# Kernel optimization log

Measured on AMD Instinct MI355X. Metric: run time of the kernel, lower is better.

Reference implementation:

```python
import jax, jax.numpy as jnp
import numpy as np

H, W = 512, 512          # output image size (RenderLayer h, w)
CHUNK = 16               # faces per scan step in the rasterizer
BIG = 1e30
EPS = 1e-8


def _edge(ax, ay, bx, by, px, py):
    # 2D edge function (signed parallelogram area)
    return (px - ax) * (by - ay) - (py - ay) * (bx - ax)


def _project(v, campos, camrot, focal, princpt):
    # v: [N,V,3] -> camera space and pixel space (x_pix, y_pix, z_cam)
    v_cam = jnp.einsum('nij,nvj->nvi', camrot, v - campos[:, None])
    z = jnp.maximum(v_cam[..., 2:3], EPS)
    xy = jnp.einsum('nij,nvj->nvi', focal, v_cam[..., :2] / z) + princpt[:, None]
    v_pix = jnp.concatenate([xy, v_cam[..., 2:3]], axis=-1)
    return v_cam, v_pix


def _rasterize(v_pix, vi):
    # Z-buffer rasterization: returns per-pixel face index (-1 = background).
    N = v_pix.shape[0]
    F = vi.shape[0]
    px = jnp.arange(W, dtype=v_pix.dtype)[None, None, None, :]
    py = jnp.arange(H, dtype=v_pix.dtype)[None, None, :, None]
    tri = v_pix[:, vi]                       # [N,F,3,3]
    nchunks = F // CHUNK
    tri_c = jnp.moveaxis(tri.reshape(N, nchunks, CHUNK, 3, 3), 1, 0)  # [nc,N,C,3,3]
    base = jnp.arange(nchunks, dtype=jnp.int32) * CHUNK

    def body(carry, xs):
        best_d, best_i = carry
        t, b0 = xs                           # t: [N,C,3,3]
        x0 = t[:, :, 0, 0][..., None, None]; y0 = t[:, :, 0, 1][..., None, None]; z0 = t[:, :, 0, 2][..., None, None]
        x1 = t[:, :, 1, 0][..., None, None]; y1 = t[:, :, 1, 1][..., None, None]; z1 = t[:, :, 1, 2][..., None, None]
        x2 = t[:, :, 2, 0][..., None, None]; y2 = t[:, :, 2, 1][..., None, None]; z2 = t[:, :, 2, 2][..., None, None]
        w0 = _edge(x1, y1, x2, y2, px, py)   # [N,C,H,W]
        w1 = _edge(x2, y2, x0, y0, px, py)
        w2 = _edge(x0, y0, x1, y1, px, py)
        area = _edge(x0, y0, x1, y1, x2, y2)
        inside = (w0 * area >= 0) & (w1 * area >= 0) & (w2 * area >= 0) & (jnp.abs(area) > EPS)
        sa = jnp.where(jnp.abs(area) > EPS, area, 1.0)
        zi = (w0 / sa) / jnp.maximum(z0, EPS) + (w1 / sa) / jnp.maximum(z1, EPS) + (w2 / sa) / jnp.maximum(z2, EPS)
        valid = inside & (z0 > EPS) & (z1 > EPS) & (z2 > EPS) & (zi > EPS)
        d = jnp.where(valid, 1.0 / jnp.maximum(zi, EPS), BIG)
        d_min = jnp.min(d, axis=1)
        i_min = jnp.argmin(d, axis=1).astype(jnp.int32) + b0
        upd = d_min < best_d
        return (jnp.where(upd, d_min, best_d), jnp.where(upd, i_min, best_i)), None

    init = (jnp.full((N, H, W), BIG, v_pix.dtype), jnp.full((N, H, W), -1, jnp.int32))
    (best_d, best_i), _ = jax.lax.scan(body, init, (tri_c, base))
    mask = best_d < BIG
    return jnp.where(mask, best_i, -1), mask


def _interp(v_pix, vt, vi, vti, index_img, mask):
    # Perspective-correct barycentric interp of depth and texcoords (interp_vert_attrs)
    safe = jnp.maximum(index_img, 0)
    f_v = vi[safe]                            # [N,H,W,3]
    f_vt = vti[safe]
    pv = jax.vmap(lambda vp, t: vp[t])(v_pix, f_v)  # [N,H,W,3,3]
    px = jnp.arange(W, dtype=v_pix.dtype)[None, None, :]
    py = jnp.arange(H, dtype=v_pix.dtype)[None, :, None]
    x0, y0 = pv[..., 0, 0], pv[..., 0, 1]
    x1, y1 = pv[..., 1, 0], pv[..., 1, 1]
    x2, y2 = pv[..., 2, 0], pv[..., 2, 1]
    w0 = _edge(x1, y1, x2, y2, px, py)
    w1 = _edge(x2, y2, x0, y0, px, py)
    w2 = _edge(x0, y0, x1, y1, px, py)
    area = _edge(x0, y0, x1, y1, x2, y2)
    sa = jnp.where(jnp.abs(area) > EPS, area, 1.0)
    b = jnp.stack([w0, w1, w2], -1) / sa[..., None]     # screen-space bary [N,H,W,3]
    z = jnp.maximum(pv[..., 2], EPS)
    bz = b / z
    zi = jnp.maximum(jnp.sum(bz, -1, keepdims=True), EPS)
    bary = jnp.where(mask[..., None], bz / zi, 0.0)     # perspective-correct bary
    depth_img = jnp.where(mask, 1.0 / zi[..., 0], 0.0)
    vt_tri = vt[f_vt]                                   # [N,H,W,3,2]
    vt_img = jnp.einsum('nhwk,nhwkc->nhwc', bary, vt_tri)
    return depth_img, bary, vt_img


def _grid_sample_border(tex, grid):
    # torch.nn.functional.grid_sample: bilinear, padding_mode='border', align_corners=False
    N, C, Ht, Wt = tex.shape
    t = jnp.moveaxis(tex, 1, -1)              # [N,Ht,Wt,C]
    ix = (grid[..., 0] + 1.0) * 0.5 * Wt - 0.5
    iy = (grid[..., 1] + 1.0) * 0.5 * Ht - 0.5
    x0 = jnp.floor(ix); y0 = jnp.floor(iy)
    fx = (ix - x0)[..., None]; fy = (iy - y0)[..., None]
    x0i = jnp.clip(x0.astype(jnp.int32), 0, Wt - 1)
    x1i = jnp.clip(x0.astype(jnp.int32) + 1, 0, Wt - 1)
    y0i = jnp.clip(y0.astype(jnp.int32), 0, Ht - 1)
    y1i = jnp.clip(y0.astype(jnp.int32) + 1, 0, Ht - 1)
    gather = jax.vmap(lambda img, y, x: img[y, x])
    v00 = gather(t, y0i, x0i); v01 = gather(t, y0i, x1i)
    v10 = gather(t, y1i, x0i); v11 = gather(t, y1i, x1i)
    out = (v00 * (1 - fx) + v01 * fx) * (1 - fy) + (v10 * (1 - fx) + v11 * fx) * fy
    return jnp.moveaxis(out, -1, 1)           # [N,C,H,W]


def setup_inputs() -> dict:
    key = jax.random.key(0)
    ks = jax.random.split(key, 6)
    N, V, F, T = 2, 4096, 2048, 4096
    xy = jax.random.uniform(ks[0], (N, V, 2), minval=-1.0, maxval=1.0)
    z = jax.random.uniform(ks[1], (N, V, 1), minval=2.0, maxval=4.0)
    v = jnp.concatenate([xy, z], -1)
    tex = jax.random.normal(ks[2], (N, 3, 1024, 1024), dtype=jnp.float32)
    vt = jax.random.uniform(ks[3], (T, 2))
    vi = jax.random.randint(ks[4], (F, 3), 0, V, dtype=jnp.int32)
    vti = jax.random.randint(ks[5], (F, 3), 0, T, dtype=jnp.int32)
    campos = jnp.zeros((N, 3), jnp.float32)
    camrot = jnp.tile(jnp.eye(3, dtype=jnp.float32)[None], (N, 1, 1))
    focal = jnp.tile(jnp.array([[512.0, 0.0], [0.0, 512.0]], jnp.float32)[None], (N, 1, 1))
    princpt = jnp.full((N, 2), 256.0, jnp.float32)
    return {"v": v, "tex": tex, "vt": vt, "vi": vi, "vti": vti,
            "campos": campos, "camrot": camrot, "focal": focal, "princpt": princpt}


def reference(v, tex, vt, vi, vti, campos, camrot, focal, princpt):
    vt = vt.at[:, 1].set(1.0 - vt[:, 1])      # flip_uvs=True buffer transform
    v_cam, v_pix = _project(v, campos, camrot, focal, princpt)
    index_img, mask = _rasterize(jax.lax.stop_gradient(v_pix), vi)
    depth_img, bary, vt_img = _interp(v_pix, vt, vi, vti, index_img, mask)
    grid = vt_img * 2.0 - 1.0                 # uv in [0,1] -> grid_sample coords
    render = _grid_sample_border(tex, grid) * mask[:, None].astype(tex.dtype)
    bary_img = jnp.moveaxis(bary, -1, 1)
    return render, mask.astype(jnp.float32), depth_img, vt_img, bary_img, index_img
```

## Files before the change

kernel.cpp:

```cpp
#include <hip/hip_runtime.h>
#include <math.h>

#define EPSD 1e-8
#define EPSF 1e-8f
#define IMG_H 512
#define IMG_W 512
#define TEX_W 1024
#define TEX_H 1024
#define REJ_SLACK 1e-3
#define FULL_THR 16.0
#define TILES_X (IMG_W / 16)
#define TILES_Y (IMG_H / 16)
#define TILES_PER_IMG (TILES_X * TILES_Y)

__global__ __launch_bounds__(256) void k_project(
    const float* __restrict__ v,
    const float* __restrict__ campos,
    const float* __restrict__ camrot,
    const float* __restrict__ focal,
    const float* __restrict__ princpt,
    double* __restrict__ vpixd,
    int N, int V) {
#pragma clang fp contract(off)
  int i = blockIdx.x * blockDim.x + threadIdx.x;
  if (i >= N * V) return;
  int n = i / V;
  const float* vv = v + (size_t)i * 3;
  double ax = (double)vv[0] - (double)campos[n * 3 + 0];
  double ay = (double)vv[1] - (double)campos[n * 3 + 1];
  double az = (double)vv[2] - (double)campos[n * 3 + 2];
  const float* R = camrot + (size_t)n * 9;
  double cx = ((double)R[0] * ax + (double)R[1] * ay) + (double)R[2] * az;
  double cy = ((double)R[3] * ax + (double)R[4] * ay) + (double)R[5] * az;
  double cz = ((double)R[6] * ax + (double)R[7] * ay) + (double)R[8] * az;
  double zz = fmax(cz, EPSD);
  double xd = cx / zz;
  double yd = cy / zz;
  const float* Fc = focal + (size_t)n * 4;
  double px = ((double)Fc[0] * xd + (double)Fc[1] * yd) + (double)princpt[n * 2 + 0];
  double py = ((double)Fc[2] * xd + (double)Fc[3] * yd) + (double)princpt[n * 2 + 1];
  vpixd[(size_t)i * 3 + 0] = px;
  vpixd[(size_t)i * 3 + 1] = py;
  vpixd[(size_t)i * 3 + 2] = cz;
}

__global__ __launch_bounds__(256) void k_setup(
    const double* __restrict__ vpixd,
    const int* __restrict__ vi,
    double2* __restrict__ tri,
    float4* __restrict__ bbox,
    int* __restrict__ counter,
    int N, int V, int F) {
#pragma clang fp contract(off)
  int i = blockIdx.x * blockDim.x + threadIdx.x;
  if (i == 0) counter[0] = 0;
  if (i >= N * F) return;
  int n = i / F;
  int f = i - n * F;
  int i0 = vi[f * 3 + 0], i1 = vi[f * 3 + 1], i2 = vi[f * 3 + 2];
  const double* p0 = vpixd + ((size_t)n * V + i0) * 3;
  const double* p1 = vpixd + ((size_t)n * V + i1) * 3;
  const double* p2 = vpixd + ((size_t)n * V + i2) * 3;
  double x0 = p0[0], y0 = p0[1], z0 = p0[2];
  double x1 = p1[0], y1 = p1[1], z1 = p1[2];
  double x2 = p2[0], y2 = p2[1], z2 = p2[2];
  double A0 = y2 - y1, B0 = x2 - x1;
  double A1 = y0 - y2, B1 = x0 - x2;
  double A2 = y1 - y0, B2 = x1 - x0;
  double area = (x2 - x0) * A2 - (y2 - y0) * B2;
  bool valid = (fabs(area) > EPSD) && (z0 > EPSD) && (z1 > EPSD) && (z2 > EPSD);
  double s = area;
  double EA0 = 0.0, EB0 = 0.0, EC0 = -1.0;
  double EA1 = 0.0, EB1 = 0.0, EC1 = -1.0;
  double EA2 = 0.0, EB2 = 0.0, EC2 = -1.0;
  double P = 0.0, Q = 0.0, S = 0.0;
  if (valid) {
    EA0 = A0 * s; EB0 = -(B0 * s); EC0 = (y1 * B0 - x1 * A0) * s;
    EA1 = A1 * s; EB1 = -(B1 * s); EC1 = (y2 * B1 - x2 * A1) * s;
    EA2 = A2 * s; EB2 = -(B2 * s); EC2 = (y0 * B2 - x0 * A2) * s;
    double s2 = s * s;
    double R0 = 1.0 / (s2 * fmax(z0, EPSD));
    double R1 = 1.0 / (s2 * fmax(z1, EPSD));
    double R2 = 1.0 / (s2 * fmax(z2, EPSD));
    P = EA0 * R0 + EA1 * R1 + EA2 * R2;
    S = EB0 * R0 + EB1 * R1 + EB2 * R2;
    Q = EC0 * R0 + EC1 * R1 + EC2 * R2;
  }
  double2* T = tri + (size_t)i * 6;
  T[0] = make_double2(EA0, EB0);
  T[1] = make_double2(EC0, EA1);
  T[2] = make_double2(EB1, EC1);
  T[3] = make_double2(EA2, EB2);
  T[4] = make_double2(EC2, P);
  T[5] = make_double2(Q, S);
  float mnx = (float)fmin(x0, fmin(x1, x2));
  float mny = (float)fmin(y0, fmin(y1, y2));
  float mxx = (float)fmax(x0, fmax(x1, x2));
  float mxy = (float)fmax(y0, fmax(y1, y2));
  bbox[i] = make_float4(mnx, mny, mxx, mxy);
}

__device__ inline void steal_to_tile(int s, int& tx, int& ty) {
  int k = (int)(__fsqrt_rn((float)s) * 0.5f);
  while (k > 0 && 4 * k * k > s) --k;
  while (4 * (k + 1) * (k + 1) <= s) ++k;
  int o = s - 4 * k * k;
  int L = 2 * k + 2;
  int x0 = TILES_X / 2 - 1 - k, y0 = TILES_Y / 2 - 1 - k;
  int side = o / (L - 1);
  int off = o - side * (L - 1);
  if (side == 0)      { tx = x0 + off;         ty = y0; }
  else if (side == 1) { tx = x0 + L - 1;       ty = y0 + off; }
  else if (side == 2) { tx = x0 + L - 1 - off; ty = y0 + L - 1; }
  else                { tx = x0;               ty = y0 + L - 1 - off; }
}

__device__ inline double rl_d(double v, int l) {
  int lo = __builtin_amdgcn_readlane(__double2loint(v), l);
  int hi = __builtin_amdgcn_readlane(__double2hiint(v), l);
  return __hiloint2double(hi, lo);
}

__global__ __launch_bounds__(256, 2) void k_raster(
    const double2* __restrict__ tri,
    const float4* __restrict__ bbox,
    int* __restrict__ counter,
    const double* __restrict__ vpixd,
    const float* __restrict__ vt,
    const int* __restrict__ vi,
    const int* __restrict__ vti,
    const float* __restrict__ tex,
    float* __restrict__ out,
    int N, int V, int F) {
#pragma clang fp contract(off)
  __shared__ __align__(16) char smem[12288];
  double* zbuf = (double*)smem;
  int* ibuf = (int*)(smem + 8192);
  __shared__ int s_steal;

  int tid = threadIdx.x;
  int w = tid >> 6, lane = tid & 63;
  int xl = lane & 15, yb = (lane >> 4) * 4;
  int FQ = (F + 3) >> 2;
  int fbeg = w * FQ;
  int fend = min(F, fbeg + FQ);
  int NR = (fend > fbeg) ? ((fend - fbeg + 63) >> 6) : 0;
  const int TOT = N * TILES_PER_IMG;
  const int HW = IMG_H * IMG_W;
  const size_t NHW = (size_t)N * HW;
  float* out_render = out;
  float* out_mask = out + 3 * NHW;
  float* out_depth = out + 4 * NHW;
  float* out_vt = out + 5 * NHW;
  float* out_bary = out + 7 * NHW;
  float* out_idx = out + 10 * NHW;

  for (;;) {
    if (tid == 0) s_steal = atomicAdd(counter, 1);
    __syncthreads();
    int s = s_steal;
    if (s >= TOT) break;
    int n = s % N;
    int q = s / N;
    int tx, ty;
    steal_to_tile(q, tx, ty);

    int x = tx * 16 + xl;
    int ytop = ty * 16;
    double px = (double)x;
    double py0 = (double)(ytop + yb);
    float tminx = (float)(tx * 16) - 0.5f;
    float tmaxx = tminx + 16.0f;
    float tminy = (float)ytop - 0.5f;
    float tmaxy = tminy + 16.0f;
    double X0 = (double)(tx * 16), X1 = X0 + 15.0;
    double Y0 = (double)ytop, Y1 = Y0 + 15.0;

    double bz[4];
    int bi[4];
#pragma unroll
    for (int r = 0; r < 4; ++r) { bz[r] = EPSD; bi[r] = -1; }

    const double2* trin = tri + (size_t)n * F * 6;
    const float4* bbn = bbox + (size_t)n * F;

    float4 bbB = make_float4(0.f, 0.f, 0.f, 0.f);
    bool bbpA = false;
    double2 A0, A1, A2, A3, A4, A5;
    if (NR > 0) {
      int t0 = fbeg + lane;
      float4 bbA;
      if (t0 < fend) bbA = bbn[t0];
      bbpA = (t0 < fend) &&
             !(bbA.z < tminx || bbA.x > tmaxx || bbA.w < tminy || bbA.y > tmaxy);
      if (bbpA) {
        const double2* T = trin + (size_t)t0 * 6;
        A0 = T[0]; A1 = T[1]; A2 = T[2]; A3 = T[3]; A4 = T[4]; A5 = T[5];
      }
      if (t0 + 64 < fend) bbB = bbn[t0 + 64];
    }
    for (int r = 0; r < NR; ++r) {
      int tbase = fbeg + (r << 6);
      bool surv = false, full = false;
      if (bbpA) {
        double xs0 = (A0.x >= 0.0) ? X1 : X0;
        double ys0 = (A0.y >= 0.0) ? Y1 : Y0;
        double w0M = fma(ys0, A0.y, fma(xs0, A0.x, A1.x));
        double xs1 = (A1.y >= 0.0) ? X1 : X0;
        double ys1 = (A2.x >= 0.0) ? Y1 : Y0;
        double w1M = fma(ys1, A2.x, fma(xs1, A1.y, A2.y));
        double xs2 = (A3.x >= 0.0) ? X1 : X0;
        double ys2 = (A3.y >= 0.0) ? Y1 : Y0;
        double w2M = fma(ys2, A3.y, fma(xs2, A3.x, A4.x));
        surv = (w0M >= -REJ_SLACK) & (w1M >= -REJ_SLACK) & (w2M >= -REJ_SLACK);
        if (surv) {
          double xn0 = (A0.x >= 0.0) ? X0 : X1;
          double yn0 = (A0.y >= 0.0) ? Y0 : Y1;
          double w0m = fma(yn0, A0.y, fma(xn0, A0.x, A1.x));
          double xn1 = (A1.y >= 0.0) ? X0 : X1;
          double yn1 = (A2.x >= 0.0) ? Y0 : Y1;
          double w1m = fma(yn1, A2.x, fma(xn1, A1.y, A2.y));
          double xn2 = (A3.x >= 0.0) ? X0 : X1;
          double yn2 = (A3.y >= 0.0) ? Y0 : Y1;
          double w2m = fma(yn2, A3.y, fma(xn2, A3.x, A4.x));
          full = (w0m >= FULL_THR) & (w1m >= FULL_THR) & (w2m >= FULL_THR);
        }
      }
      unsigned long long m = __ballot(surv);
      unsigned long long mf = __ballot(surv && full);
      int tn1 = tbase + 64 + lane;
      bool bbpB = (tn1 < fend) &&
                  !(bbB.z < tminx || bbB.x > tmaxx || bbB.w < tminy || bbB.y > tmaxy);
      double2 B0, B1, B2, B3, B4, B5;
      if (bbpB) {
        const double2* T = trin + (size_t)tn1 * 6;
        B0 = T[0]; B1 = T[1]; B2 = T[2]; B3 = T[3]; B4 = T[4]; B5 = T[5];
      }
      if (tn1 + 64 < fend) bbB = bbn[tn1 + 64];
      while (m) {
        int src = (int)__builtin_ctzll(m);
        m &= m - 1;
        int ti = tbase + src;
        double P = rl_d(A4.y, src);
        double Qq = rl_d(A5.x, src);
        double S = rl_d(A5.y, src);
        double uu = fma(px, P, Qq);
        if ((mf >> src) & 1ull) {
          double py = py0;
#pragma unroll
          for (int rr = 0; rr < 4; ++rr) {
            double zi = fma(py, S, uu);
            if (zi > bz[rr]) { bz[rr] = zi; bi[rr] = ti; }
            py += 1.0;
          }
        } else {
          double EA0 = rl_d(A0.x, src), EB0 = rl_d(A0.y, src);
          double EC0 = rl_d(A1.x, src), EA1 = rl_d(A1.y, src);
          double EB1 = rl_d(A2.x, src), EC1 = rl_d(A2.y, src);
          double EA2 = rl_d(A3.x, src), EB2 = rl_d(A3.y, src);
          double EC2 = rl_d(A4.x, src);
          double q0 = fma(px, EA0, EC0);
          double q1 = fma(px, EA1, EC1);
          double q2 = fma(px, EA2, EC2);
          double py = py0;
#pragma unroll
          for (int rr = 0; rr < 4; ++rr) {
            double W0 = fma(py, EB0, q0);
            double W1 = fma(py, EB1, q1);
            double W2 = fma(py, EB2, q2);
            double zi = fma(py, S, uu);
            int msk = (__double2hiint(W0) | __double2hiint(W1) |
                       __double2hiint(W2)) >> 31;
            zi = __hiloint2double(__double2hiint(zi) | msk, __double2loint(zi));
            if (zi > bz[rr]) { bz[rr] = zi; bi[rr] = ti; }
            py += 1.0;
          }
        }
      }
      A0 = B0; A1 = B1; A2 = B2; A3 = B3; A4 = B4; A5 = B5;
      bbpA = bbpB;
    }

    __syncthreads();
#pragma unroll
    for (int r = 0; r < 4; ++r) {
      int pix = (yb + r) * 16 + xl;
      zbuf[w * 256 + pix] = bz[r];
      ibuf[w * 256 + pix] = bi[r];
    }
    __syncthreads();
    {
      int pix = tid;
      double z = zbuf[pix];
      int i = ibuf[pix];
#pragma unroll
      for (int qq = 1; qq < 4; ++qq) {
        double zq = zbuf[qq * 256 + pix];
        int iq = ibuf[qq * 256 + pix];
        bool take = (zq > z) || ((zq == z) && ((unsigned)iq < (unsigned)i));
        if (take) { z = zq; i = iq; }
      }
      int yloc = pix >> 4, xloc = pix & 15;
      int y = ytop + yloc;
      int xg = tx * 16 + xloc;
      int p = y * IMG_W + xg;
      size_t gid = (size_t)n * HW + p;
      out_idx[gid] = (float)i;

      int idx = i;
      if (idx < 0) {
        for (int c = 0; c < 3; ++c) out_render[(size_t)(n * 3 + c) * HW + p] = 0.0f;
        out_mask[gid] = 0.0f;
        out_depth[gid] = 0.0f;
        out_vt[(size_t)gid * 2 + 0] = 0.0f;
        out_vt[(size_t)gid * 2 + 1] = 0.0f;
        for (int k = 0; k < 3; ++k) out_bary[(size_t)(n * 3 + k) * HW + p] = 0.0f;
      } else {
        int f0 = vi[idx * 3 + 0], f1 = vi[idx * 3 + 1], f2 = vi[idx * 3 + 2];
        int t0i = vti[idx * 3 + 0], t1i = vti[idx * 3 + 1], t2i = vti[idx * 3 + 2];
        const double* pv0 = vpixd + ((size_t)n * V + f0) * 3;
        const double* pv1 = vpixd + ((size_t)n * V + f1) * 3;
        const double* pv2 = vpixd + ((size_t)n * V + f2) * 3;
        float x0 = (float)pv0[0], y0 = (float)pv0[1], z0 = (float)pv0[2];
        float x1 = (float)pv1[0], y1 = (float)pv1[1], z1 = (float)pv1[2];
        float x2 = (float)pv2[0], y2 = (float)pv2[1], z2 = (float)pv2[2];
        float pxf = (float)xg, pyf = (float)y;
        float w0 = (pxf - x1) * (y2 - y1) - (pyf - y1) * (x2 - x1);
        float w1 = (pxf - x2) * (y0 - y2) - (pyf - y2) * (x0 - x2);
        float w2 = (pxf - x0) * (y1 - y0) - (pyf - y0) * (x1 - x0);
        float area = (x2 - x0) * (y1 - y0) - (y2 - y0) * (x1 - x0);
        float sa = (fabsf(area) > EPSF) ? area : 1.0f;
        float b0 = w0 / sa, b1 = w1 / sa, b2 = w2 / sa;
        float zz0 = fmaxf(z0, EPSF), zz1 = fmaxf(z1, EPSF), zz2 = fmaxf(z2, EPSF);
        float bz0 = b0 / zz0, bz1 = b1 / zz1, bz2 = b2 / zz2;
        float zi = fmaxf((bz0 + bz1) + bz2, EPSF);
        float r0 = bz0 / zi, r1 = bz1 / zi, r2 = bz2 / zi;
        float depth = 1.0f / zi;
        float u0 = vt[(size_t)t0i * 2 + 0], q0 = 1.0f - vt[(size_t)t0i * 2 + 1];
        float u1 = vt[(size_t)t1i * 2 + 0], q1 = 1.0f - vt[(size_t)t1i * 2 + 1];
        float u2 = vt[(size_t)t2i * 2 + 0], q2 = 1.0f - vt[(size_t)t2i * 2 + 1];
        float vtx = (r0 * u0 + r1 * u1) + r2 * u2;
        float vty = (r0 * q0 + r1 * q1) + r2 * q2;
        float gx = vtx * 2.0f - 1.0f;
        float gy = vty * 2.0f - 1.0f;
        float ix = ((gx + 1.0f) * 0.5f) * (float)TEX_W - 0.5f;
        float iy = ((gy + 1.0f) * 0.5f) * (float)TEX_H - 0.5f;
        float x0f = floorf(ix), y0f = floorf(iy);
        float fx = ix - x0f, fy = iy - y0f;
        int x0i = min(max((int)x0f, 0), TEX_W - 1);
        int x1i = min(max((int)x0f + 1, 0), TEX_W - 1);
        int y0i = min(max((int)y0f, 0), TEX_H - 1);
        int y1i = min(max((int)y0f + 1, 0), TEX_H - 1);
        float omfx = 1.0f - fx, omfy = 1.0f - fy;
        for (int c = 0; c < 3; ++c) {
          const float* tc = tex + (size_t)(n * 3 + c) * TEX_H * TEX_W;
          float v00 = tc[(size_t)y0i * TEX_W + x0i];
          float v01 = tc[(size_t)y0i * TEX_W + x1i];
          float v10 = tc[(size_t)y1i * TEX_W + x0i];
          float v11 = tc[(size_t)y1i * TEX_W + x1i];
          float o = (v00 * omfx + v01 * fx) * omfy + (v10 * omfx + v11 * fx) * fy;
          out_render[(size_t)(n * 3 + c) * HW + p] = o;
        }
        out_mask[gid] = 1.0f;
        out_depth[gid] = depth;
        out_vt[(size_t)gid * 2 + 0] = vtx;
        out_vt[(size_t)gid * 2 + 1] = vty;
        out_bary[(size_t)(n * 3 + 0) * HW + p] = r0;
        out_bary[(size_t)(n * 3 + 1) * HW + p] = r1;
        out_bary[(size_t)(n * 3 + 2) * HW + p] = r2;
      }
    }
  }
}

extern "C" void kernel_launch(void* const* d_in, const int* in_sizes, int n_in,
                              void* d_out, int out_size, void* d_ws, size_t ws_size,
                              hipStream_t stream) {
  const float* v = (const float*)d_in[0];
  const float* tex = (const float*)d_in[1];
  const float* vt = (const float*)d_in[2];
  const int* vi = (const int*)d_in[3];
  const int* vti = (const int*)d_in[4];
  const float* campos = (const float*)d_in[5];
  const float* camrot = (const float*)d_in[6];
  const float* focal = (const float*)d_in[7];
  const float* princpt = (const float*)d_in[8];
  int N = in_sizes[5] / 3;
  int V = in_sizes[0] / (3 * N);
  int F = in_sizes[3] / 3;

  char* wp = (char*)d_ws;
  double* vpixd = (double*)wp;
  wp += sizeof(double) * (size_t)N * V * 3;
  double2* tri = (double2*)wp;
  wp += sizeof(double2) * (size_t)N * F * 6;
  float4* bbox = (float4*)wp;
  wp += sizeof(float4) * (size_t)N * F;
  int* counter = (int*)wp;

  int nv = N * V;
  k_project<<<(nv + 255) / 256, 256, 0, stream>>>(v, campos, camrot, focal,
                                                  princpt, vpixd, N, V);
  int nf = N * F;
  k_setup<<<(nf + 255) / 256, 256, 0, stream>>>(vpixd, vi, tri, bbox, counter,
                                                N, V, F);
  int nblk = 1024;
  int tot = N * TILES_PER_IMG;
  if (nblk > tot) nblk = tot;
  k_raster<<<nblk, 256, 0, stream>>>(tri, bbox, counter, vpixd, vt, vi, vti,
                                     tex, (float*)d_out, N, V, F);
}
```

Before: 168.0 us.

## Enlarge raster tiles to 32x16 with center-out separable tile ordering

Raster tiles grow from 16x16 to 32x16. Each lane now covers 8 rows instead of 4, and the shared-memory z/index merge buffers are doubled to match. This amortises per-triangle work (bbox test, triangle loads, readlane broadcasts) over more pixels per tile. The spiral tile ordering is replaced with a simpler center-out permutation applied separately to each axis, and the block count rises. The cost is more registers per thread and more shared memory, and larger tiles overlap more triangles, so more partial-coverage work is done per tile.

```diff
diff --git a/kernel.cpp b/kernel.cpp
--- a/kernel.cpp
+++ b/kernel.cpp
@@ -9,8 +9,10 @@
 #define TEX_H 1024
 #define REJ_SLACK 1e-3
 #define FULL_THR 16.0
-#define TILES_X (IMG_W / 16)
-#define TILES_Y (IMG_H / 16)
+#define TILE_W 32
+#define TILE_H 16
+#define TILES_X (IMG_W / TILE_W)
+#define TILES_Y (IMG_H / TILE_H)
 #define TILES_PER_IMG (TILES_X * TILES_Y)
 
 __global__ __launch_bounds__(256) void k_project(
@@ -100,19 +102,9 @@
   bbox[i] = make_float4(mnx, mny, mxx, mxy);
 }
 
-__device__ inline void steal_to_tile(int s, int& tx, int& ty) {
-  int k = (int)(__fsqrt_rn((float)s) * 0.5f);
-  while (k > 0 && 4 * k * k > s) --k;
-  while (4 * (k + 1) * (k + 1) <= s) ++k;
-  int o = s - 4 * k * k;
-  int L = 2 * k + 2;
-  int x0 = TILES_X / 2 - 1 - k, y0 = TILES_Y / 2 - 1 - k;
-  int side = o / (L - 1);
-  int off = o - side * (L - 1);
-  if (side == 0)      { tx = x0 + off;         ty = y0; }
-  else if (side == 1) { tx = x0 + L - 1;       ty = y0 + off; }
-  else if (side == 2) { tx = x0 + L - 1 - off; ty = y0 + L - 1; }
-  else                { tx = x0;               ty = y0 + L - 1 - off; }
+__device__ inline int perm_co(int i, int n) {
+  int h = n >> 1;
+  return (i & 1) ? (h - 1 - (i >> 1)) : (h + (i >> 1));
 }
 
 __device__ inline double rl_d(double v, int l) {
@@ -133,14 +125,14 @@
     float* __restrict__ out,
     int N, int V, int F) {
 #pragma clang fp contract(off)
-  __shared__ __align__(16) char smem[12288];
+  __shared__ __align__(16) char smem[24576];
   double* zbuf = (double*)smem;
-  int* ibuf = (int*)(smem + 8192);
+  int* ibuf = (int*)(smem + 16384);
   __shared__ int s_steal;
 
   int tid = threadIdx.x;
   int w = tid >> 6, lane = tid & 63;
-  int xl = lane & 15, yb = (lane >> 4) * 4;
+  int xl = lane & 31, yb = (lane >> 5) * 8;
   int FQ = (F + 3) >> 2;
   int fbeg = w * FQ;
   int fend = min(F, fbeg + FQ);
@@ -162,24 +154,24 @@
     if (s >= TOT) break;
     int n = s % N;
     int q = s / N;
-    int tx, ty;
-    steal_to_tile(q, tx, ty);
-
-    int x = tx * 16 + xl;
-    int ytop = ty * 16;
+    int ty = perm_co(q / TILES_X, TILES_Y);
+    int tx = perm_co(q % TILES_X, TILES_X);
+
+    int x = tx * TILE_W + xl;
+    int ytop = ty * TILE_H;
     double px = (double)x;
     double py0 = (double)(ytop + yb);
-    float tminx = (float)(tx * 16) - 0.5f;
-    float tmaxx = tminx + 16.0f;
+    float tminx = (float)(tx * TILE_W) - 0.5f;
+    float tmaxx = tminx + (float)TILE_W;
     float tminy = (float)ytop - 0.5f;
-    float tmaxy = tminy + 16.0f;
-    double X0 = (double)(tx * 16), X1 = X0 + 15.0;
-    double Y0 = (double)ytop, Y1 = Y0 + 15.0;
-
-    double bz[4];
-    int bi[4];
-#pragma unroll
-    for (int r = 0; r < 4; ++r) { bz[r] = EPSD; bi[r] = -1; }
+    float tmaxy = tminy + (float)TILE_H;
+    double X0 = (double)(tx * TILE_W), X1 = X0 + (double)(TILE_W - 1);
+    double Y0 = (double)ytop, Y1 = Y0 + (double)(TILE_H - 1);
+
+    double bz[8];
+    int bi[8];
+#pragma unroll
+    for (int r = 0; r < 8; ++r) { bz[r] = EPSD; bi[r] = -1; }
 
     const double2* trin = tri + (size_t)n * F * 6;
     const float4* bbn = bbox + (size_t)n * F;
@@ -248,7 +240,7 @@
         if ((mf >> src) & 1ull) {
           double py = py0;
 #pragma unroll
-          for (int rr = 0; rr < 4; ++rr) {
+          for (int rr = 0; rr < 8; ++rr) {
             double zi = fma(py, S, uu);
             if (zi > bz[rr]) { bz[rr] = zi; bi[rr] = ti; }
             py += 1.0;
@@ -264,7 +256,7 @@
           double q2 = fma(px, EA2, EC2);
           double py = py0;
 #pragma unroll
-          for (int rr = 0; rr < 4; ++rr) {
+          for (int rr = 0; rr < 8; ++rr) {
             double W0 = fma(py, EB0, q0);
             double W1 = fma(py, EB1, q1);
             double W2 = fma(py, EB2, q2);
@@ -283,26 +275,27 @@
 
     __syncthreads();
 #pragma unroll
-    for (int r = 0; r < 4; ++r) {
-      int pix = (yb + r) * 16 + xl;
-      zbuf[w * 256 + pix] = bz[r];
-      ibuf[w * 256 + pix] = bi[r];
+    for (int r = 0; r < 8; ++r) {
+      int pix = (yb + r) * TILE_W + xl;
+      zbuf[w * 512 + pix] = bz[r];
+      ibuf[w * 512 + pix] = bi[r];
     }
     __syncthreads();
-    {
-      int pix = tid;
+#pragma unroll
+    for (int k = 0; k < 2; ++k) {
+      int pix = tid + k * 256;
       double z = zbuf[pix];
       int i = ibuf[pix];
 #pragma unroll
       for (int qq = 1; qq < 4; ++qq) {
-        double zq = zbuf[qq * 256 + pix];
-        int iq = ibuf[qq * 256 + pix];
+        double zq = zbuf[qq * 512 + pix];
+        int iq = ibuf[qq * 512 + pix];
         bool take = (zq > z) || ((zq == z) && ((unsigned)iq < (unsigned)i));
         if (take) { z = zq; i = iq; }
       }
-      int yloc = pix >> 4, xloc = pix & 15;
+      int yloc = pix >> 5, xloc = pix & 31;
       int y = ytop + yloc;
-      int xg = tx * 16 + xloc;
+      int xg = tx * TILE_W + xloc;
       int p = y * IMG_W + xg;
       size_t gid = (size_t)n * HW + p;
       out_idx[gid] = (float)i;
@@ -314,7 +307,7 @@
         out_depth[gid] = 0.0f;
         out_vt[(size_t)gid * 2 + 0] = 0.0f;
         out_vt[(size_t)gid * 2 + 1] = 0.0f;
-        for (int k = 0; k < 3; ++k) out_bary[(size_t)(n * 3 + k) * HW + p] = 0.0f;
+        for (int kk = 0; kk < 3; ++kk) out_bary[(size_t)(n * 3 + kk) * HW + p] = 0.0f;
       } else {
         int f0 = vi[idx * 3 + 0], f1 = vi[idx * 3 + 1], f2 = vi[idx * 3 + 2];
         int t0i = vti[idx * 3 + 0], t1i = vti[idx * 3 + 1], t2i = vti[idx * 3 + 2];
@@ -404,7 +397,7 @@
   int nf = N * F;
   k_setup<<<(nf + 255) / 256, 256, 0, stream>>>(vpixd, vi, tri, bbox, counter,
                                                 N, V, F);
-  int nblk = 1024;
+  int nblk = 1536;
   int tot = N * TILES_PER_IMG;
   if (nblk > tot) nblk = tot;
   k_raster<<<nblk, 256, 0, stream>>>(tri, bbox, counter, vpixd, vt, vi, vti,
```

New measurement: 195.7 us. 16.5% more time.
